# Performance work log

Hardware: AMD Instinct MI355X
Metric: run time of the kernel (lower is better)

The kernel has to match this reference:

```python
import jax, jax.numpy as jnp
import numpy as np


def setup_inputs() -> dict:
    key = jax.random.key(0)
    ks = jax.random.split(key, 6)
    b, h, w, m, d = 8, 32, 32, 8, 64
    c = m * d
    return {
        "x": jax.random.normal(ks[0], (b, h, w, c), jnp.float32),
        "qkv_w": jax.random.normal(ks[1], (d, 3 * d), jnp.float32) * np.float32(1.0 / np.sqrt(d)),
        "qkv_b": jnp.zeros((3 * d,), jnp.float32),
        # HeNormal over (2h-1)^2 scalar table
        "pos_emb": jax.random.normal(ks[2], ((2 * h - 1) ** 2,), jnp.float32) * np.float32(np.sqrt(2.0 / (2 * h - 1) ** 2)),
        "ht_w": jax.random.normal(ks[3], (c, c), jnp.float32) * np.float32(1.0 / np.sqrt(c)),
        "ht_b": jnp.zeros((c,), jnp.float32),
    }


def _rel_pos_idx(h):
    # Static Swin-style 2D relative position index, shape (h*h, h*h)
    coords = jnp.arange(h)
    base = coords[None, :] - coords[:, None]          # base[a, b] = b - a
    horiz = jnp.tile(base, (h, h))                    # (h^2, h^2)
    vert = jnp.repeat(jnp.repeat(base, h, axis=0), h, axis=1)
    return (2 * h - 1) * (vert + h - 1) + (horiz + h - 1)


def reference(x, qkv_w, qkv_b, pos_emb, ht_w, ht_b):
    b, h, w, c = x.shape
    d = qkv_w.shape[0]
    m = c // d
    hw = h * w
    # split channels into heads: (b, m, hw, d)
    xh = x.reshape(b, h, w, m, d).transpose(0, 3, 1, 2, 4).reshape(b, m, hw, d)
    # 1x1 conv == per-position linear, then channel layout (d, 3) as in the TF reshape
    qkv = (xh @ qkv_w + qkv_b).reshape(b, m, hw, d, 3)
    q, k, v = qkv[..., 0], qkv[..., 1], qkv[..., 2]
    q = q / jnp.sqrt(jnp.float32(d))
    att = jnp.einsum('bmic,bmjc->bmij', q, k)         # (b, m, hw, hw)
    att = att + pos_emb[_rel_pos_idx(h)]              # bias shared across batch & heads
    att = jax.nn.softmax(att, axis=-1)
    out = jnp.einsum('bmij,bmjc->bmic', att, v)       # (b, m, hw, d)
    out = out.reshape(b, m, h, w, d).transpose(0, 2, 3, 1, 4).reshape(b, h, w, c)
    return out @ ht_w + ht_b
```

## Files before the change

### kernel.cpp

```cpp
#include <hip/hip_runtime.h>

#define Dd 64
#define Cc 512
#define HW 1024
#define BM 64
#define LOG2E 1.44269504f

typedef __attribute__((ext_vector_type(8))) short bf16x8;
typedef __attribute__((ext_vector_type(4))) short bf16x4;
typedef __attribute__((ext_vector_type(4))) float f32x4;

__device__ __forceinline__ unsigned short f2bf(float f) {
  unsigned int u = __builtin_bit_cast(unsigned int, f);
  u += 0x7fffu + ((u >> 16) & 1u);
  return (unsigned short)(u >> 16);
}

__device__ __forceinline__ unsigned int pack2(float lo, float hi) {
  return (unsigned int)f2bf(lo) | ((unsigned int)f2bf(hi) << 16);
}

__device__ __forceinline__ int swz(int row, int cb) {
  return row * 128 + (cb ^ ((row & 7) << 4));
}

__global__ __launch_bounds__(256, 2) void qkv_kernel(
    const float* __restrict__ x, const float* __restrict__ w,
    const float* __restrict__ bqkv,
    unsigned short* __restrict__ Q, unsigned short* __restrict__ K,
    unsigned short* __restrict__ Vt) {
  __shared__ unsigned short Wt[192 * 64];
  __shared__ float bl[192];
  char* WtB = (char*)Wt;
  int t = threadIdx.x, lane = t & 63, wv = t >> 6;
  int c = lane & 15, r4 = lane >> 4;
  int bm = blockIdx.x >> 2;
  int chunk0 = (blockIdx.x & 3) * 256;
  int bb = bm >> 3, mm = bm & 7;

  for (int idx = t; idx < 12288; idx += 256) {
    int k = idx / 192, col = idx - (idx / 192) * 192;
    int d3 = col / 3, which = col - d3 * 3;
    int np = which * 64 + d3;
    float v = w[idx];
    if (which == 0) v *= 0.125f;
    *(unsigned short*)(WtB + np * 128 + ((k * 2) ^ ((np & 7) << 4))) = f2bf(v);
  }
  if (t < 192) {
    int d3 = t / 3, which = t - d3 * 3;
    float bvv = bqkv[t];
    if (which == 0) bvv *= 0.125f;
    bl[which * 64 + d3] = bvv;
  }
  __syncthreads();

  bf16x8 af[12][2];
#pragma unroll
  for (int nf = 0; nf < 12; ++nf) {
    int row = nf * 16 + c, sw = (row & 7) << 4;
#pragma unroll
    for (int kc = 0; kc < 2; ++kc)
      af[nf][kc] = *(const bf16x8*)(WtB + row * 128 + ((kc * 64 + r4 * 16) ^ sw));
  }
  f32x4 bseed[12];
#pragma unroll
  for (int nf = 0; nf < 12; ++nf)
    bseed[nf] = *(const f32x4*)&bl[nf * 16 + r4 * 4];

  for (int pg = 0; pg < 4; ++pg) {
    int pos = chunk0 + pg * 64 + wv * 16 + c;
    const float* xr = x + (size_t)(bb * HW + pos) * Cc + mm * Dd;
    bf16x8 xb[2];
#pragma unroll
    for (int kc = 0; kc < 2; ++kc) {
      f32x4 lo = *(const f32x4*)(xr + kc * 32 + r4 * 8);
      f32x4 hi = *(const f32x4*)(xr + kc * 32 + r4 * 8 + 4);
      union { unsigned int u[4]; bf16x8 b; } cv;
      cv.u[0] = pack2(lo[0], lo[1]);
      cv.u[1] = pack2(lo[2], lo[3]);
      cv.u[2] = pack2(hi[0], hi[1]);
      cv.u[3] = pack2(hi[2], hi[3]);
      xb[kc] = cv.b;
    }
    f32x4 acc[12];
#pragma unroll
    for (int nf = 0; nf < 12; ++nf) {
      acc[nf] = bseed[nf];
      acc[nf] = __builtin_amdgcn_mfma_f32_16x16x32_bf16(af[nf][0], xb[0], acc[nf], 0, 0, 0);
      acc[nf] = __builtin_amdgcn_mfma_f32_16x16x32_bf16(af[nf][1], xb[1], acc[nf], 0, 0, 0);
    }
    size_t obase = ((size_t)bm * HW + pos) * Dd;
#pragma unroll
    for (int nf = 0; nf < 8; ++nf) {
      unsigned int d0 = pack2(acc[nf][0], acc[nf][1]);
      unsigned int d1 = pack2(acc[nf][2], acc[nf][3]);
      unsigned long long wd = (unsigned long long)d0 | ((unsigned long long)d1 << 32);
      unsigned short* dst = (nf < 4) ? Q : K;
      *(unsigned long long*)(dst + obase + (nf & 3) * 16 + r4 * 4) = wd;
    }
#pragma unroll
    for (int nf = 8; nf < 12; ++nf) {
#pragma unroll
      for (int reg = 0; reg < 4; ++reg) {
        int d = (nf - 8) * 16 + r4 * 4 + reg;
        Vt[((size_t)bm * Dd + d) * HW + pos] = f2bf(acc[nf][reg]);
      }
    }
  }
}

__global__ __launch_bounds__(256, 4) void attn_kernel(
    const unsigned short* __restrict__ Q, const unsigned short* __restrict__ K,
    const unsigned short* __restrict__ Vt, const float* __restrict__ pe,
    unsigned short* __restrict__ O) {
  __shared__ unsigned short Kt[2][64 * 64];
  __shared__ unsigned short Vl[2][64 * 64];
  __shared__ unsigned short Pl[4][1024];
  char* PlB = (char*)Pl;
  int t = threadIdx.x, lane = t & 63, wv = t >> 6;
  int c = lane & 15, r4 = lane >> 4;
  int swzid = (blockIdx.x & 7) * 128 + (blockIdx.x >> 3);
  int bm = swzid >> 4;
  int i0 = (swzid & 15) * 64;

  const unsigned short* Qb = Q + ((size_t)bm * HW + i0 + wv * 16) * Dd;
  bf16x8 qb[2];
#pragma unroll
  for (int kc = 0; kc < 2; ++kc)
    qb[kc] = *(const bf16x8*)(Qb + c * Dd + kc * 32 + r4 * 8);

  int ibase = i0 + wv * 16;
  int yi = ibase >> 5, xib = ibase & 31;
  int hb = 63 * (31 - yi) + 31 - xib - c + r4 * 4;

  f32x4 oacc[4];
  float m_run = -1e30f, l_run = 0.f;
#pragma unroll
  for (int nf = 0; nf < 4; ++nf) oacc[nf] = {0.f, 0.f, 0.f, 0.f};

  const unsigned short* Kg = K + (size_t)bm * HW * Dd;
  const unsigned short* Vg = Vt + (size_t)bm * Dd * HW;
  char* pb = PlB + wv * 2048 + c * 128;
  int swp = (c & 7) << 4;
  int srow = t >> 3, sc8 = t & 7;

  bf16x8 kreg[2], vreg[2];
  auto issue = [&](int j0) {
#pragma unroll
    for (int rep = 0; rep < 2; ++rep) {
      int row = srow + rep * 32;
      kreg[rep] = *(const bf16x8*)(Kg + (size_t)(j0 + row) * Dd + sc8 * 8);
      vreg[rep] = *(const bf16x8*)(Vg + (size_t)row * HW + j0 + sc8 * 8);
    }
  };
  auto stage = [&](int buf) {
#pragma unroll
    for (int rep = 0; rep < 2; ++rep) {
      int row = srow + rep * 32;
      *(bf16x8*)((char*)Kt[buf] + swz(row, sc8 * 16)) = kreg[rep];
      *(bf16x8*)((char*)Vl[buf] + swz(row, sc8 * 16)) = vreg[rep];
    }
  };

  issue(0);
  stage(0);
  issue(64);
  __syncthreads();

  int cur = 0;
  for (int jt = 0; jt < 16; ++jt) {
    int j0 = jt * 64;
    if (jt < 15) {
      stage(cur ^ 1);
      if (jt < 14) issue(j0 + 128);
    }
    char* KtB = (char*)Kt[cur];
    char* VtB = (char*)Vl[cur];

    f32x4 sacc[4];
    int tb = hb + 63 * (j0 >> 5);
#pragma unroll
    for (int jf = 0; jf < 4; ++jf) {
      int o = tb + (jf >> 1) * 63 + (jf & 1) * 16;
      sacc[jf] = {pe[o], pe[o + 1], pe[o + 2], pe[o + 3]};
    }
#pragma unroll
    for (int jf = 0; jf < 4; ++jf) {
      int row = jf * 16 + c, sw = (row & 7) << 4;
      bf16x8 kb0 = *(const bf16x8*)(KtB + row * 128 + ((r4 * 16) ^ sw));
      bf16x8 kb1 = *(const bf16x8*)(KtB + row * 128 + ((64 + r4 * 16) ^ sw));
      sacc[jf] = __builtin_amdgcn_mfma_f32_16x16x32_bf16(kb0, qb[0], sacc[jf], 0, 0, 0);
      sacc[jf] = __builtin_amdgcn_mfma_f32_16x16x32_bf16(kb1, qb[1], sacc[jf], 0, 0, 0);
    }
    float mx = fmaxf(
        fmaxf(fmaxf(fmaxf(sacc[0][0], sacc[0][1]), fmaxf(sacc[0][2], sacc[0][3])),
              fmaxf(fmaxf(sacc[1][0], sacc[1][1]), fmaxf(sacc[1][2], sacc[1][3]))),
        fmaxf(fmaxf(fmaxf(sacc[2][0], sacc[2][1]), fmaxf(sacc[2][2], sacc[2][3])),
              fmaxf(fmaxf(sacc[3][0], sacc[3][1]), fmaxf(sacc[3][2], sacc[3][3]))));
    mx = fmaxf(mx, __shfl_xor(mx, 16));
    mx = fmaxf(mx, __shfl_xor(mx, 32));
    if (!__all(mx <= m_run + 8.f)) {
      float mnew = fmaxf(m_run, mx);
      float sc = __builtin_amdgcn_exp2f((m_run - mnew) * LOG2E);
      m_run = mnew;
      l_run *= sc;
#pragma unroll
      for (int nf = 0; nf < 4; ++nf) oacc[nf] *= sc;
    }
    float ml = m_run * LOG2E;
    float ps = 0.f;
#pragma unroll
    for (int jf = 0; jf < 4; ++jf)
#pragma unroll
      for (int r = 0; r < 4; ++r) {
        float p = __builtin_amdgcn_exp2f(fmaf(sacc[jf][r], LOG2E, -ml));
        sacc[jf][r] = p;
        ps += p;
      }
    ps += __shfl_xor(ps, 16);
    ps += __shfl_xor(ps, 32);
    l_run += ps;
#pragma unroll
    for (int jf = 0; jf < 4; ++jf) {
      unsigned int w0 = pack2(sacc[jf][0], sacc[jf][1]);
      unsigned int w1 = pack2(sacc[jf][2], sacc[jf][3]);
      unsigned long long wd = (unsigned long long)w0 | ((unsigned long long)w1 << 32);
      *(unsigned long long*)(pb + ((jf * 32 + r4 * 8) ^ swp)) = wd;
    }
#pragma unroll
    for (int jk = 0; jk < 2; ++jk) {
      bf16x8 pa = *(const bf16x8*)(pb + ((jk * 64 + r4 * 16) ^ swp));
#pragma unroll
      for (int nf = 0; nf < 4; ++nf) {
        int row = nf * 16 + c, sw = (row & 7) << 4;
        bf16x8 vb = *(const bf16x8*)(VtB + row * 128 + ((jk * 64 + r4 * 16) ^ sw));
        oacc[nf] = __builtin_amdgcn_mfma_f32_16x16x32_bf16(vb, pa, oacc[nf], 0, 0, 0);
      }
    }
    if (jt < 15) {
      __syncthreads();
      cur ^= 1;
    }
  }

  __syncthreads();
  char* zone = ((wv < 2) ? (char*)Kt[0] : (char*)Vl[0]) + (wv & 1) * 4096;
  float inv = 1.f / l_run;
  int swc = (c & 7) << 4;
#pragma unroll
  for (int nf = 0; nf < 4; ++nf) {
    unsigned int d0 = pack2(oacc[nf][0] * inv, oacc[nf][1] * inv);
    unsigned int d1 = pack2(oacc[nf][2] * inv, oacc[nf][3] * inv);
    unsigned long long wd = (unsigned long long)d0 | ((unsigned long long)d1 << 32);
    *(unsigned long long*)(zone + c * 128 + ((nf * 32 + r4 * 8) ^ swc)) = wd;
  }
  __syncthreads();
  int rrow = lane >> 2, dq = lane & 3;
  int swr = (rrow & 7) << 4;
  size_t obase = ((size_t)bm * HW + i0 + wv * 16 + rrow) * Dd + dq * 16;
#pragma unroll
  for (int p = 0; p < 2; ++p) {
    bf16x8 vv = *(const bf16x8*)(zone + rrow * 128 + ((dq * 32 + p * 16) ^ swr));
    *(bf16x8*)(O + obase + p * 8) = vv;
  }
}

__global__ __launch_bounds__(256, 2) void proj_kernel(
    const unsigned short* __restrict__ O, const float* __restrict__ W,
    const float* __restrict__ bias, float* __restrict__ out) {
  __shared__ unsigned short Bt[2][64 * 64];
  int t = threadIdx.x, lane = t & 63, wv = t >> 6;
  int rb = blockIdx.x >> 3, n0 = (blockIdx.x & 7) * 64;
  int row0 = rb * 128;
  int b = row0 >> 10, pos0 = row0 & 1023;
  int c = lane & 15, r4 = lane >> 4;
  int nt = t & 15, kt = t >> 4;

  f32x4 acc[2][4];
#pragma unroll
  for (int g = 0; g < 2; ++g)
#pragma unroll
    for (int nf = 0; nf < 4; ++nf) acc[g][nf] = {0.f, 0.f, 0.f, 0.f};

  f32x4 wreg[4];
  bf16x8 aA[4], aB[4];

  auto issueW = [&](int m) {
#pragma unroll
    for (int r = 0; r < 4; ++r)
      wreg[r] = *(const f32x4*)(W + (size_t)(m * 64 + kt * 4 + r) * Cc + n0 + nt * 4);
  };
  auto issueA = [&](bf16x8 (&ar)[4], int m) {
    const unsigned short* Ob = O + ((size_t)(b * 8 + m) * HW + pos0) * Dd;
#pragma unroll
    for (int g = 0; g < 2; ++g)
#pragma unroll
      for (int kc = 0; kc < 2; ++kc)
        ar[g * 2 + kc] = *(const bf16x8*)(Ob + (size_t)(wv * 32 + g * 16 + c) * Dd +
                                          kc * 32 + r4 * 8);
  };
  auto stageB = [&](int buf) {
    char* BtB = (char*)Bt[buf];
#pragma unroll
    for (int e = 0; e < 4; ++e) {
      bf16x4 bt = {(short)f2bf(wreg[0][e]), (short)f2bf(wreg[1][e]),
                   (short)f2bf(wreg[2][e]), (short)f2bf(wreg[3][e])};
      *(bf16x4*)(BtB + swz(nt * 4 + e, kt * 8)) = bt;
    }
  };

  issueW(0);
  issueA(aA, 0);
  stageB(0);
  issueW(1);
  issueA(aB, 1);
  __syncthreads();

  int cur = 0;
  for (int m = 0; m < 8; ++m) {
    if (m < 7) {
      stageB(cur ^ 1);
      if (m < 6) issueW(m + 2);
    }
    char* BtB = (char*)Bt[cur];
    bf16x8* ar = (m & 1) ? aB : aA;
#pragma unroll
    for (int kc = 0; kc < 2; ++kc) {
#pragma unroll
      for (int nf = 0; nf < 4; ++nf) {
        bf16x8 bb = *(const bf16x8*)(BtB + swz(nf * 16 + c, kc * 64 + r4 * 16));
        acc[0][nf] = __builtin_amdgcn_mfma_f32_16x16x32_bf16(ar[kc], bb, acc[0][nf], 0, 0, 0);
        acc[1][nf] = __builtin_amdgcn_mfma_f32_16x16x32_bf16(ar[2 + kc], bb, acc[1][nf], 0, 0, 0);
      }
    }
    if (m < 6) issueA((m & 1) ? aB : aA, m + 2);
    if (m < 7) {
      __syncthreads();
      cur ^= 1;
    }
  }

  float bv[4];
#pragma unroll
  for (int nf = 0; nf < 4; ++nf) bv[nf] = bias[n0 + nf * 16 + c];
#pragma unroll
  for (int g = 0; g < 2; ++g) {
#pragma unroll
    for (int reg = 0; reg < 4; ++reg) {
      int row = row0 + wv * 32 + g * 16 + r4 * 4 + reg;
#pragma unroll
      for (int nf = 0; nf < 4; ++nf)
        out[(size_t)row * Cc + n0 + nf * 16 + c] = acc[g][nf][reg] + bv[nf];
    }
  }
}

extern "C" void kernel_launch(void* const* d_in, const int* in_sizes, int n_in,
                              void* d_out, int out_size, void* d_ws, size_t ws_size,
                              hipStream_t stream) {
  const float* x      = (const float*)d_in[0];
  const float* qkv_w  = (const float*)d_in[1];
  const float* qkv_b  = (const float*)d_in[2];
  const float* pos_emb= (const float*)d_in[3];
  const float* ht_w   = (const float*)d_in[4];
  const float* ht_b   = (const float*)d_in[5];
  float* out = (float*)d_out;

  const size_t NQ = (size_t)BM * HW * Dd;
  unsigned short* Qw  = (unsigned short*)d_ws;
  unsigned short* Kw  = Qw + NQ;
  unsigned short* Vtw = Kw + NQ;
  unsigned short* Ow  = Vtw + NQ;

  hipLaunchKernelGGL(qkv_kernel, dim3(256), dim3(256), 0, stream,
                     x, qkv_w, qkv_b, Qw, Kw, Vtw);
  hipLaunchKernelGGL(attn_kernel, dim3(1024), dim3(256), 0, stream,
                     Qw, Kw, Vtw, pos_emb, Ow);
  hipLaunchKernelGGL(proj_kernel, dim3(512), dim3(256), 0, stream,
                     Ow, ht_w, ht_b, out);
}
```

Baseline: 71.65 us.

## Load K fragments directly from global into registers, dropping K LDS staging

```diff
diff --git a/kernel.cpp b/kernel.cpp
--- a/kernel.cpp
+++ b/kernel.cpp
@@ -113,7 +113,6 @@
     const unsigned short* __restrict__ Q, const unsigned short* __restrict__ K,
     const unsigned short* __restrict__ Vt, const float* __restrict__ pe,
     unsigned short* __restrict__ O) {
-  __shared__ unsigned short Kt[2][64 * 64];
   __shared__ unsigned short Vl[2][64 * 64];
   __shared__ unsigned short Pl[4][1024];
   char* PlB = (char*)Pl;
@@ -144,39 +143,32 @@
   int swp = (c & 7) << 4;
   int srow = t >> 3, sc8 = t & 7;
 
-  bf16x8 kreg[2], vreg[2];
-  auto issue = [&](int j0) {
+  bf16x8 vreg[2];
+  auto issueV = [&](int j0) {
 #pragma unroll
     for (int rep = 0; rep < 2; ++rep) {
       int row = srow + rep * 32;
-      kreg[rep] = *(const bf16x8*)(Kg + (size_t)(j0 + row) * Dd + sc8 * 8);
       vreg[rep] = *(const bf16x8*)(Vg + (size_t)row * HW + j0 + sc8 * 8);
     }
   };
-  auto stage = [&](int buf) {
+  auto stageV = [&](int buf) {
 #pragma unroll
     for (int rep = 0; rep < 2; ++rep) {
       int row = srow + rep * 32;
-      *(bf16x8*)((char*)Kt[buf] + swz(row, sc8 * 16)) = kreg[rep];
       *(bf16x8*)((char*)Vl[buf] + swz(row, sc8 * 16)) = vreg[rep];
     }
   };
-
-  issue(0);
-  stage(0);
-  issue(64);
-  __syncthreads();
-
-  int cur = 0;
-  for (int jt = 0; jt < 16; ++jt) {
-    int j0 = jt * 64;
-    if (jt < 15) {
-      stage(cur ^ 1);
-      if (jt < 14) issue(j0 + 128);
-    }
-    char* KtB = (char*)Kt[cur];
-    char* VtB = (char*)Vl[cur];
-
+  auto loadK = [&](bf16x8 (&kf)[8], int j0) {
+#pragma unroll
+    for (int jf = 0; jf < 4; ++jf) {
+      const unsigned short* kr = Kg + (size_t)(j0 + jf * 16 + c) * Dd + r4 * 8;
+      kf[jf * 2 + 0] = *(const bf16x8*)(kr);
+      kf[jf * 2 + 1] = *(const bf16x8*)(kr + 32);
+    }
+  };
+
+  auto COMPUTE = [&](bf16x8 (&kf)[8], int buf, int j0) {
+    char* VtB = (char*)Vl[buf];
     f32x4 sacc[4];
     int tb = hb + 63 * (j0 >> 5);
 #pragma unroll
@@ -186,11 +178,8 @@
     }
 #pragma unroll
     for (int jf = 0; jf < 4; ++jf) {
-      int row = jf * 16 + c, sw = (row & 7) << 4;
-      bf16x8 kb0 = *(const bf16x8*)(KtB + row * 128 + ((r4 * 16) ^ sw));
-      bf16x8 kb1 = *(const bf16x8*)(KtB + row * 128 + ((64 + r4 * 16) ^ sw));
-      sacc[jf] = __builtin_amdgcn_mfma_f32_16x16x32_bf16(kb0, qb[0], sacc[jf], 0, 0, 0);
-      sacc[jf] = __builtin_amdgcn_mfma_f32_16x16x32_bf16(kb1, qb[1], sacc[jf], 0, 0, 0);
+      sacc[jf] = __builtin_amdgcn_mfma_f32_16x16x32_bf16(kf[jf * 2 + 0], qb[0], sacc[jf], 0, 0, 0);
+      sacc[jf] = __builtin_amdgcn_mfma_f32_16x16x32_bf16(kf[jf * 2 + 1], qb[1], sacc[jf], 0, 0, 0);
     }
     float mx = fmaxf(
         fmaxf(fmaxf(fmaxf(sacc[0][0], sacc[0][1]), fmaxf(sacc[0][2], sacc[0][3])),
@@ -237,14 +226,38 @@
         oacc[nf] = __builtin_amdgcn_mfma_f32_16x16x32_bf16(vb, pa, oacc[nf], 0, 0, 0);
       }
     }
-    if (jt < 15) {
+  };
+
+  bf16x8 kA[8], kB[8];
+  loadK(kA, 0);
+  issueV(0);
+  stageV(0);
+  issueV(64);
+  __syncthreads();
+
+  int cur = 0;
+  for (int jt2 = 0; jt2 < 8; ++jt2) {
+    int j0e = jt2 * 128, j0o = j0e + 64;
+    loadK(kB, j0o);
+    stageV(cur ^ 1);
+    if (jt2 < 7) issueV(j0o + 64);
+    COMPUTE(kA, cur, j0e);
+    __syncthreads();
+    cur ^= 1;
+    if (jt2 < 7) {
+      loadK(kA, j0e + 128);
+      stageV(cur ^ 1);
+      issueV(j0e + 192);
+      COMPUTE(kB, cur, j0o);
       __syncthreads();
       cur ^= 1;
-    }
-  }
-
-  __syncthreads();
-  char* zone = ((wv < 2) ? (char*)Kt[0] : (char*)Vl[0]) + (wv & 1) * 4096;
+    } else {
+      COMPUTE(kB, cur, j0o);
+    }
+  }
+
+  __syncthreads();
+  char* zone = (char*)Vl[wv >> 1] + (wv & 1) * 4096;
   float inv = 1.f / l_run;
   int swc = (c & 7) << 4;
 #pragma unroll
```

New measurement: 118.8 us. +65.8%, slower.
